# Optimization experiments

Hardware: AMD Instinct MI355X
Metric: run time of the kernel (lower is better)

## Reference

```python
import math
import jax, jax.numpy as jnp
import numpy as np

B, S, D, H = 2, 2048, 1024, 16
HD = D // H
I = 3752  # round(1024 * 11/3 / 8) * 8, per GluMLP default
EPS = 1e-6


def _alibi_bias(nheads, n):
    # AlibiPostionEmbedding: slopes (power-of-2 formula) * -1, times |i-j|
    start = 2.0 ** (-(2.0 ** (-(math.log2(nheads) - 3))))
    slopes = np.array([start * start ** i for i in range(nheads)], dtype=np.float64) * -1.0
    pos = np.arange(n)
    rel = np.abs(pos[None, :] - pos[:, None])  # [n, n]
    return jnp.asarray(slopes[:, None, None] * rel[None, :, :], dtype=jnp.float32)


def rmsnorm(h, w):
    h32 = h.astype(jnp.float32)
    var = jnp.mean(h32 * h32, axis=-1, keepdims=True)
    return (w * (h32 * jax.lax.rsqrt(var + EPS))).astype(h.dtype)


def setup_inputs() -> dict:
    key = jax.random.key(0)
    ks = jax.random.split(key, 16)
    sd = 1.0 / math.sqrt(D)
    si = 1.0 / math.sqrt(I)
    rn = lambda k, shape, s: jax.random.normal(k, shape, jnp.float32) * s
    return {
        "x": rn(ks[0], (B, S, D), 1.0),
        "wq": rn(ks[1], (D, D), sd), "bq": rn(ks[2], (D,), 0.02),
        "wk": rn(ks[3], (D, D), sd), "bk": rn(ks[4], (D,), 0.02),
        "wv": rn(ks[5], (D, D), sd), "bv": rn(ks[6], (D,), 0.02),
        "wo": rn(ks[7], (D, D), sd), "bo": rn(ks[8], (D,), 0.02),
        "w_gate": rn(ks[9], (D, I), sd),
        "w_up": rn(ks[10], (D, I), sd),
        "w_down": rn(ks[11], (I, D), si),
        "ln1_w": jnp.ones((D,), jnp.float32),
        "ln2_w": jnp.ones((D,), jnp.float32),
        "attn_bias": _alibi_bias(H, S),                       # [H, S, S]
        "tgt_mask": jnp.triu(jnp.ones((S, S), bool), 1),      # causal, True = masked
        "key_padding_mask": jnp.zeros((B, S), bool),          # True = padded
    }


def reference(x, wq, bq, wk, bk, wv, bv, wo, bo, w_gate, w_up, w_down,
              ln1_w, ln2_w, attn_bias, tgt_mask, key_padding_mask):
    # ---- TransformerEncoderLayer.forward (eval mode: dropout = identity) ----
    residual = x
    h = rmsnorm(x, ln1_w)
    # MultiheadAttention with ALiBi bias + fused bool masks
    q = (h @ wq + bq).reshape(B, S, H, HD)
    k = (h @ wk + bk).reshape(B, S, H, HD)
    v = (h @ wv + bv).reshape(B, S, H, HD)
    scores = jnp.einsum("bqhd,bkhd->bhqk", q, k) * (HD ** -0.5)  # [B,H,S,S]
    scores = scores + attn_bias[None]
    mask = tgt_mask[None, :, :] | key_padding_mask[:, None, :]   # [B,S,S]
    scores = jnp.where(mask[:, None, :, :], -jnp.inf, scores)
    probs = jax.nn.softmax(scores, axis=-1)
    attn = jnp.einsum("bhqk,bkhd->bqhd", probs, v).reshape(B, S, D)
    attn = attn @ wo + bo
    residual = attn + residual
    # GluMLP (SwiGLU)
    h2 = rmsnorm(residual, ln2_w)
    mlp = (jax.nn.silu(h2 @ w_gate) * (h2 @ w_up)) @ w_down
    return mlp + residual
```

## Files before the change

kernel.cpp:

```cpp
#include <hip/hip_runtime.h>
#include <hip/hip_bf16.h>
#include <cmath>

typedef __bf16 bf16_t;
typedef __bf16 bf16x8 __attribute__((ext_vector_type(8)));
typedef short  s16x8  __attribute__((ext_vector_type(8)));
typedef float  f32x4  __attribute__((ext_vector_type(4)));

static constexpr int Bn  = 2;
static constexpr int Sn  = 2048;
static constexpr int Dn  = 1024;
static constexpr int Hn  = 16;
static constexpr int In  = 3752;
static constexpr int Mn  = Bn * Sn;
static constexpr int Ipad = 3840;

__device__ __forceinline__ void cp16(const bf16_t* g, bf16_t* l) {
  __builtin_amdgcn_global_load_lds(
      (const __attribute__((address_space(1))) unsigned int*)g,
      (__attribute__((address_space(3))) unsigned int*)l, 16, 0, 0);
}

__global__ __launch_bounds__(256) void k_transpose(const float* __restrict__ in,
                                                   bf16_t* __restrict__ out,
                                                   int R, int C) {
  __shared__ float tile[32][33];
  const int c0 = blockIdx.x * 32, r0 = blockIdx.y * 32;
  const int tx = threadIdx.x & 31, ty = threadIdx.x >> 5;
#pragma unroll
  for (int e = 0; e < 4; ++e) {
    int r = r0 + ty + e * 8, c = c0 + tx;
    if (r < R && c < C) tile[ty + e * 8][tx] = in[(size_t)r * C + c];
  }
  __syncthreads();
#pragma unroll
  for (int e = 0; e < 4; ++e) {
    int c = c0 + ty + e * 8, r = r0 + tx;
    if (r < R && c < C) out[(size_t)c * R + r] = (bf16_t)tile[tx][ty + e * 8];
  }
}

__global__ __launch_bounds__(256) void k_rmsnorm(const float* __restrict__ in,
                                                 const float* __restrict__ w,
                                                 bf16_t* __restrict__ out) {
  const int row = blockIdx.x;
  const int tid = threadIdx.x;
  const float* ip = in + (size_t)row * Dn;
  float v[4];
  float ss = 0.f;
#pragma unroll
  for (int e = 0; e < 4; ++e) {
    v[e] = ip[tid + e * 256];
    ss += v[e] * v[e];
  }
  for (int off = 32; off > 0; off >>= 1) ss += __shfl_down(ss, off);
  __shared__ float red[4];
  if ((tid & 63) == 0) red[tid >> 6] = ss;
  __syncthreads();
  float tot = red[0] + red[1] + red[2] + red[3];
  float sc = rsqrtf(tot * (1.0f / Dn) + 1e-6f);
  bf16_t* op = out + (size_t)row * Dn;
#pragma unroll
  for (int e = 0; e < 4; ++e) {
    int idx = tid + e * 256;
    op[idx] = (bf16_t)(w[idx] * v[e] * sc);
  }
}

__global__ __launch_bounds__(256) void k_gemm64(
    const bf16_t* __restrict__ A, const bf16_t* __restrict__ Bt,
    const float* __restrict__ bias, const float* __restrict__ resid,
    float* __restrict__ outf, int N, int K, int lda, int ldb) {
  __shared__ bf16_t As[64 * 64];
  __shared__ bf16_t Bs[128 * 64];
  const int m0 = blockIdx.x * 64, n0 = blockIdx.y * 128;
  const int tid = threadIdx.x;
  const int lane = tid & 63, wid = tid >> 6;
  const int wc = wid * 32;
  const int l15 = lane & 15, quad = lane >> 4;
  const int sw = l15 & 7;
  const int srow_lo = lane >> 3, pchunk = lane & 7;

  f32x4 acc[4][2];
  const f32x4 z4 = {0.f, 0.f, 0.f, 0.f};
#pragma unroll
  for (int i = 0; i < 4; ++i)
#pragma unroll
    for (int j = 0; j < 2; ++j) acc[i][j] = z4;

  for (int k0 = 0; k0 < K; k0 += 64) {
#pragma unroll
    for (int c = 0; c < 2; ++c) {
      const int r = (wid * 2 + c) * 8 + srow_lo;
      const int gc = pchunk ^ (r & 7);
      cp16(A + (size_t)(m0 + r) * lda + k0 + gc * 8, As + (wid * 2 + c) * 512);
    }
#pragma unroll
    for (int c = 0; c < 4; ++c) {
      const int r = (wid * 4 + c) * 8 + srow_lo;
      const int gc = pchunk ^ (r & 7);
      cp16(Bt + (size_t)(n0 + r) * ldb + k0 + gc * 8, Bs + (wid * 4 + c) * 512);
    }
    __syncthreads();
#pragma unroll
    for (int kh = 0; kh < 2; ++kh) {
      const int ph = ((kh * 4 + quad) ^ sw) * 8;
      bf16x8 af[4], bfr[2];
#pragma unroll
      for (int i = 0; i < 4; ++i)
        af[i] = *(const bf16x8*)(As + (i * 16 + l15) * 64 + ph);
#pragma unroll
      for (int j = 0; j < 2; ++j)
        bfr[j] = *(const bf16x8*)(Bs + (wc + j * 16 + l15) * 64 + ph);
#pragma unroll
      for (int i = 0; i < 4; ++i)
#pragma unroll
        for (int j = 0; j < 2; ++j)
          acc[i][j] = __builtin_amdgcn_mfma_f32_16x16x32_bf16(af[i], bfr[j], acc[i][j], 0, 0, 0);
    }
    __syncthreads();
  }

#pragma unroll
  for (int i = 0; i < 4; ++i)
#pragma unroll
    for (int j = 0; j < 2; ++j) {
      const int col = n0 + wc + j * 16 + l15;
      const float bval = bias ? bias[col] : 0.f;
#pragma unroll
      for (int r = 0; r < 4; ++r) {
        const int row = m0 + i * 16 + quad * 4 + r;
        const size_t idx = (size_t)row * N + col;
        outf[idx] = acc[i][j][r] + bval + (resid ? resid[idx] : 0.f);
      }
    }
}

__global__ __launch_bounds__(256) void k_gemm_qkv(
    const bf16_t* __restrict__ A, const bf16_t* __restrict__ Bt,
    const float* __restrict__ bq, const float* __restrict__ bk,
    const float* __restrict__ bv,
    bf16_t* __restrict__ qk, bf16_t* __restrict__ vt) {
  __shared__ bf16_t As[128 * 64];
  __shared__ bf16_t Bs[128 * 64];
  const int m0 = blockIdx.x * 128, n0 = blockIdx.y * 128;
  const int tid = threadIdx.x;
  const int lane = tid & 63, wid = tid >> 6;
  const int wr = (wid >> 1) * 64, wc = (wid & 1) * 64;
  const int l15 = lane & 15, quad = lane >> 4;
  const int sw = l15 & 7;
  const int srow_lo = lane >> 3, pchunk = lane & 7;

  f32x4 acc[4][4];
  const f32x4 z4 = {0.f, 0.f, 0.f, 0.f};
#pragma unroll
  for (int i = 0; i < 4; ++i)
#pragma unroll
    for (int j = 0; j < 4; ++j) acc[i][j] = z4;

  for (int k0 = 0; k0 < Dn; k0 += 64) {
#pragma unroll
    for (int c = 0; c < 4; ++c) {
      const int r = (wid * 4 + c) * 8 + srow_lo;
      const int gc = pchunk ^ (r & 7);
      cp16(A  + (size_t)(m0 + r) * Dn + k0 + gc * 8, As + (wid * 4 + c) * 512);
      cp16(Bt + (size_t)(n0 + r) * Dn + k0 + gc * 8, Bs + (wid * 4 + c) * 512);
    }
    __syncthreads();
#pragma unroll
    for (int kh = 0; kh < 2; ++kh) {
      bf16x8 af[4], bfr[4];
      const int ph = ((kh * 4 + quad) ^ sw) * 8;
#pragma unroll
      for (int i = 0; i < 4; ++i)
        af[i] = *(const bf16x8*)(As + (wr + i * 16 + l15) * 64 + ph);
#pragma unroll
      for (int j = 0; j < 4; ++j)
        bfr[j] = *(const bf16x8*)(Bs + (wc + j * 16 + l15) * 64 + ph);
#pragma unroll
      for (int i = 0; i < 4; ++i)
#pragma unroll
        for (int j = 0; j < 4; ++j)
          acc[i][j] = __builtin_amdgcn_mfma_f32_16x16x32_bf16(af[i], bfr[j], acc[i][j], 0, 0, 0);
    }
    __syncthreads();
  }

#pragma unroll
  for (int i = 0; i < 4; ++i)
#pragma unroll
    for (int j = 0; j < 4; ++j) {
      const int col = n0 + wc + j * 16 + l15;
      const int sel = col >> 10;
      const float bval = (sel == 0) ? bq[col] : (sel == 1) ? bk[col - 1024] : bv[col - 2048];
#pragma unroll
      for (int r = 0; r < 4; ++r) {
        const int row = m0 + wr + i * 16 + quad * 4 + r;
        const float v = acc[i][j][r] + bval;
        if (sel < 2) {
          qk[(size_t)row * 2048 + col] = (bf16_t)v;
        } else {
          const int dd = col & 63, hh = (col >> 6) & 15;
          const int bb = row >> 11, ss = row & 2047;
          vt[(size_t)((bb * 16 + hh) * 64 + dd) * 2048 + ss] = (bf16_t)v;
        }
      }
    }
}

__global__ __launch_bounds__(256) void k_gemm_gateup(
    const bf16_t* __restrict__ A, const bf16_t* __restrict__ Bg,
    const bf16_t* __restrict__ Bu, bf16_t* __restrict__ out, int N, int ldo) {
  __shared__ bf16_t As[128 * 64];
  __shared__ bf16_t Gs[128 * 64];
  __shared__ bf16_t Us[128 * 64];
  const int m0 = blockIdx.x * 128, n0 = blockIdx.y * 128;
  const int tid = threadIdx.x;
  const int lane = tid & 63, wid = tid >> 6;
  const int wr = (wid >> 1) * 64, wc = (wid & 1) * 64;
  const int l15 = lane & 15, quad = lane >> 4;
  const int sw = l15 & 7;
  const int srow_lo = lane >> 3, pchunk = lane & 7;

  f32x4 accg[4][4], accu[4][4];
  const f32x4 z4 = {0.f, 0.f, 0.f, 0.f};
#pragma unroll
  for (int i = 0; i < 4; ++i)
#pragma unroll
    for (int j = 0; j < 4; ++j) { accg[i][j] = z4; accu[i][j] = z4; }

  for (int k0 = 0; k0 < Dn; k0 += 64) {
#pragma unroll
    for (int c = 0; c < 4; ++c) {
      const int r = (wid * 4 + c) * 8 + srow_lo;
      const int gc = pchunk ^ (r & 7);
      const int nb = min(n0 + r, N - 1);
      cp16(A  + (size_t)(m0 + r) * Dn + k0 + gc * 8, As + (wid * 4 + c) * 512);
      cp16(Bg + (size_t)nb * Dn + k0 + gc * 8, Gs + (wid * 4 + c) * 512);
      cp16(Bu + (size_t)nb * Dn + k0 + gc * 8, Us + (wid * 4 + c) * 512);
    }
    __syncthreads();
#pragma unroll
    for (int kh = 0; kh < 2; ++kh) {
      bf16x8 af[4], gf[4], uf[4];
      const int ph = ((kh * 4 + quad) ^ sw) * 8;
#pragma unroll
      for (int i = 0; i < 4; ++i)
        af[i] = *(const bf16x8*)(As + (wr + i * 16 + l15) * 64 + ph);
#pragma unroll
      for (int j = 0; j < 4; ++j) {
        gf[j] = *(const bf16x8*)(Gs + (wc + j * 16 + l15) * 64 + ph);
        uf[j] = *(const bf16x8*)(Us + (wc + j * 16 + l15) * 64 + ph);
      }
#pragma unroll
      for (int i = 0; i < 4; ++i)
#pragma unroll
        for (int j = 0; j < 4; ++j) {
          accg[i][j] = __builtin_amdgcn_mfma_f32_16x16x32_bf16(af[i], gf[j], accg[i][j], 0, 0, 0);
          accu[i][j] = __builtin_amdgcn_mfma_f32_16x16x32_bf16(af[i], uf[j], accu[i][j], 0, 0, 0);
        }
    }
    __syncthreads();
  }

#pragma unroll
  for (int i = 0; i < 4; ++i)
#pragma unroll
    for (int j = 0; j < 4; ++j) {
      const int col = n0 + wc + j * 16 + l15;
#pragma unroll
      for (int r = 0; r < 4; ++r) {
        const int row = m0 + wr + i * 16 + quad * 4 + r;
        const float g = accg[i][j][r];
        const float u = accu[i][j][r];
        const float sl = g / (1.f + expf(-g));
        out[(size_t)row * ldo + col] = (col < N) ? (bf16_t)(sl * u) : (bf16_t)0.f;
      }
    }
}

__global__ __launch_bounds__(256) void k_attn(
    const bf16_t* __restrict__ qk, const bf16_t* __restrict__ vt,
    bf16_t* __restrict__ Ob) {
  const int qt = (int)gridDim.x - 1 - (int)blockIdx.x;
  const int h  = blockIdx.y;
  const int b  = blockIdx.z;
  constexpr int LDK = 72;
  constexpr int LDP = 76;
  __shared__ bf16_t Ks[64 * LDK];
  __shared__ bf16_t Vt[64 * LDK];
  __shared__ bf16_t Ps[4][16 * LDP];

  const int tid  = threadIdx.x;
  const int lane = tid & 63, w = tid >> 6;
  const int l15  = lane & 15, quad = lane >> 4;

  constexpr float L2E = 1.4426950408889634f;
  const float slopeL = -exp2f(-0.5f * (float)(h + 1)) * L2E;

  const int qrow_frag = qt * 64 + w * 16 + l15;
  const size_t qbase = (size_t)(b * Sn + qrow_frag) * 2048 + h * 64;
  bf16x8 aq0 = *(const bf16x8*)(qk + qbase + quad * 8);
  bf16x8 aq1 = *(const bf16x8*)(qk + qbase + 32 + quad * 8);
#pragma unroll
  for (int e = 0; e < 8; ++e) {
    aq0[e] = (bf16_t)((float)aq0[e] * 0.125f);
    aq1[e] = (bf16_t)((float)aq1[e] * 0.125f);
  }

  const int qrow0 = qt * 64 + w * 16 + quad * 4;
  float Atr[4][4];
#pragma unroll
  for (int t = 0; t < 4; ++t)
#pragma unroll
    for (int rr = 0; rr < 4; ++rr)
      Atr[t][rr] = slopeL * (float)(qrow0 + rr - (t * 16 + l15));
  const float kstepL = slopeL * 64.f;

  f32x4 o[4], lacc;
  const f32x4 z4 = {0.f, 0.f, 0.f, 0.f};
#pragma unroll
  for (int dt = 0; dt < 4; ++dt) o[dt] = z4;
  lacc = z4;
  bf16x8 ones;
#pragma unroll
  for (int e = 0; e < 8; ++e) ones[e] = (bf16_t)1.0f;

  const int r = tid >> 2, c0e = (tid & 3) * 16;
  const size_t kbase = (size_t)(b * Sn + r) * 2048 + 1024 + h * 64 + c0e;
  const size_t vbase = (size_t)((b * 16 + h) * 64 + r) * 2048 + c0e;

  s16x8 kr0 = *(const s16x8*)(qk + kbase);
  s16x8 kr1 = *(const s16x8*)(qk + kbase + 8);
  s16x8 vr0 = *(const s16x8*)(vt + vbase);
  s16x8 vr1 = *(const s16x8*)(vt + vbase + 8);

  const int nkt = qt + 1;
  for (int kt = 0; kt < nkt; ++kt) {
    __syncthreads();
    *(s16x8*)(Ks + r * LDK + c0e)     = kr0;
    *(s16x8*)(Ks + r * LDK + c0e + 8) = kr1;
    *(s16x8*)(Vt + r * LDK + c0e)     = vr0;
    *(s16x8*)(Vt + r * LDK + c0e + 8) = vr1;
    __syncthreads();
    if (kt + 1 < nkt) {
      const size_t gkn = kbase + (size_t)(kt + 1) * (64 * 2048);
      kr0 = *(const s16x8*)(qk + gkn);
      kr1 = *(const s16x8*)(qk + gkn + 8);
      const size_t gvn = vbase + (size_t)(kt + 1) * 64;
      vr0 = *(const s16x8*)(vt + gvn);
      vr1 = *(const s16x8*)(vt + gvn + 8);
    }

    f32x4 s[4];
#pragma unroll
    for (int t = 0; t < 4; ++t) s[t] = z4;
#pragma unroll
    for (int t = 0; t < 4; ++t) {
      bf16x8 bk0 = *(const bf16x8*)(Ks + (t * 16 + l15) * LDK + quad * 8);
      bf16x8 bk1 = *(const bf16x8*)(Ks + (t * 16 + l15) * LDK + 32 + quad * 8);
      s[t] = __builtin_amdgcn_mfma_f32_16x16x32_bf16(aq0, bk0, s[t], 0, 0, 0);
      s[t] = __builtin_amdgcn_mfma_f32_16x16x32_bf16(aq1, bk1, s[t], 0, 0, 0);
    }

    const float ko = kstepL * (float)kt;
    const bool diag = (kt == qt);
#pragma unroll
    for (int t = 0; t < 4; ++t) {
      const int j = kt * 64 + t * 16 + l15;
#pragma unroll
      for (int rr = 0; rr < 4; ++rr) {
        float v2 = fmaf(s[t][rr], L2E, Atr[t][rr] - ko);
        if (diag && j > qrow0 + rr) v2 = -3.0e38f;
        Ps[w][(quad * 4 + rr) * LDP + t * 16 + l15] = (bf16_t)exp2f(v2);
      }
    }

#pragma unroll
    for (int kh = 0; kh < 2; ++kh) {
      bf16x8 pa = *(const bf16x8*)(Ps[w] + l15 * LDP + kh * 32 + quad * 8);
      lacc = __builtin_amdgcn_mfma_f32_16x16x32_bf16(pa, ones, lacc, 0, 0, 0);
#pragma unroll
      for (int dt = 0; dt < 4; ++dt) {
        bf16x8 bv = *(const bf16x8*)(Vt + (dt * 16 + l15) * LDK + kh * 32 + quad * 8);
        o[dt] = __builtin_amdgcn_mfma_f32_16x16x32_bf16(pa, bv, o[dt], 0, 0, 0);
      }
    }
  }

#pragma unroll
  for (int rr = 0; rr < 4; ++rr) {
    const float inv = 1.f / lacc[rr];
    bf16_t* op = Ob + ((size_t)(b * Sn + qrow0 + rr) * Hn + h) * 64;
#pragma unroll
    for (int dt = 0; dt < 4; ++dt)
      op[dt * 16 + l15] = (bf16_t)(o[dt][rr] * inv);
  }
}

extern "C" void kernel_launch(void* const* d_in, const int* in_sizes, int n_in,
                              void* d_out, int out_size, void* d_ws, size_t ws_size,
                              hipStream_t stream) {
  (void)in_sizes; (void)n_in; (void)out_size; (void)ws_size;
  const float* x   = (const float*)d_in[0];
  const float* wq  = (const float*)d_in[1];
  const float* bq  = (const float*)d_in[2];
  const float* wk_ = (const float*)d_in[3];
  const float* bk  = (const float*)d_in[4];
  const float* wv  = (const float*)d_in[5];
  const float* bv  = (const float*)d_in[6];
  const float* wo  = (const float*)d_in[7];
  const float* bo  = (const float*)d_in[8];
  const float* wg  = (const float*)d_in[9];
  const float* wu  = (const float*)d_in[10];
  const float* wd  = (const float*)d_in[11];
  const float* ln1 = (const float*)d_in[12];
  const float* ln2 = (const float*)d_in[13];

  char* base = (char*)d_ws;
  const size_t MiB = 1024 * 1024;
  bf16_t* h1     = (bf16_t*)(base);
  bf16_t* wqkvT  = (bf16_t*)(base + 8 * MiB);
  bf16_t* qkb    = (bf16_t*)(base + 16 * MiB);
  float*  res1   = (float*) (base + 16 * MiB);
  bf16_t* vt     = (bf16_t*)(base + 32 * MiB);
  bf16_t* mlp    = (bf16_t*)(base + 40 * MiB);
  bf16_t* wgT    = h1;
  bf16_t* woT    = wqkvT;
  bf16_t* wuT    = wqkvT;
  bf16_t* wdT    = vt;
  bf16_t* attnb  = (bf16_t*)d_out;
  bf16_t* h2     = (bf16_t*)d_out;

  const dim3 blk(256);
  const dim3 gT(Dn / 32, Dn / 32);

  k_rmsnorm<<<dim3(Mn), blk, 0, stream>>>(x, ln1, h1);

  k_transpose<<<gT, blk, 0, stream>>>(wq,  wqkvT, Dn, Dn);
  k_transpose<<<gT, blk, 0, stream>>>(wk_, wqkvT + (size_t)Dn * Dn, Dn, Dn);
  k_transpose<<<gT, blk, 0, stream>>>(wv,  wqkvT + 2 * (size_t)Dn * Dn, Dn, Dn);

  k_gemm_qkv<<<dim3(Mn / 128, 3072 / 128), blk, 0, stream>>>(h1, wqkvT, bq, bk, bv, qkb, vt);

  k_attn<<<dim3(Sn / 64, Hn, Bn), blk, 0, stream>>>(qkb, vt, attnb);

  k_transpose<<<gT, blk, 0, stream>>>(wo, woT, Dn, Dn);
  k_gemm64<<<dim3(Mn / 64, Dn / 128), blk, 0, stream>>>(
      attnb, woT, bo, x, res1, Dn, Dn, Dn, Dn);

  k_rmsnorm<<<dim3(Mn), blk, 0, stream>>>(res1, ln2, h2);

  k_transpose<<<dim3((In + 31) / 32, Dn / 32), blk, 0, stream>>>(wg, wgT, Dn, In);
  k_transpose<<<dim3((In + 31) / 32, Dn / 32), blk, 0, stream>>>(wu, wuT, Dn, In);
  k_transpose<<<dim3(Dn / 32, (In + 31) / 32), blk, 0, stream>>>(wd, wdT, In, Dn);

  k_gemm_gateup<<<dim3(Mn / 128, Ipad / 128), blk, 0, stream>>>(
      h2, wgT, wuT, mlp, In, Ipad);

  k_gemm64<<<dim3(Mn / 64, Dn / 128), blk, 0, stream>>>(
      mlp, wdT, nullptr, res1, (float*)d_out, Dn, Ipad, Ipad, In);
}
```

Measured before the change: 743.9 us.

## Batch weight transposes, store V row-major, and widen attention query tile to 128

All seven weight transposes are merged into one launch over a 3D grid, with separate workspace buffers so they no longer alias. The QKV GEMM now writes a plain row-major [M,3072] buffer instead of scattering V into a transposed layout, and the attention kernel transposes V into shared memory itself. Each attention block now handles 128 query rows (two 16-row groups per wave), so every K/V tile loaded is reused twice as much, at the cost of more registers, half as many blocks, and scalar strided LDS writes for the V transpose. The merged transpose grid also launches many blocks that exit early.

```diff
diff --git a/kernel.cpp b/kernel.cpp
--- a/kernel.cpp
+++ b/kernel.cpp
@@ -21,22 +21,25 @@
       (__attribute__((address_space(3))) unsigned int*)l, 16, 0, 0);
 }
 
-__global__ __launch_bounds__(256) void k_transpose(const float* __restrict__ in,
-                                                   bf16_t* __restrict__ out,
-                                                   int R, int C) {
+struct TransJob  { const float* src; bf16_t* dst; int R, C; };
+struct TransJobs { TransJob j[7]; };
+
+__global__ __launch_bounds__(256) void k_transpose_all(TransJobs jobs) {
+  const TransJob jb = jobs.j[blockIdx.z];
+  const int c0 = blockIdx.x * 32, r0 = blockIdx.y * 32;
+  if (c0 >= jb.C || r0 >= jb.R) return;
   __shared__ float tile[32][33];
-  const int c0 = blockIdx.x * 32, r0 = blockIdx.y * 32;
   const int tx = threadIdx.x & 31, ty = threadIdx.x >> 5;
 #pragma unroll
   for (int e = 0; e < 4; ++e) {
     int r = r0 + ty + e * 8, c = c0 + tx;
-    if (r < R && c < C) tile[ty + e * 8][tx] = in[(size_t)r * C + c];
+    if (r < jb.R && c < jb.C) tile[ty + e * 8][tx] = jb.src[(size_t)r * jb.C + c];
   }
   __syncthreads();
 #pragma unroll
   for (int e = 0; e < 4; ++e) {
     int c = c0 + ty + e * 8, r = r0 + tx;
-    if (r < R && c < C) out[(size_t)c * R + r] = (bf16_t)tile[tx][ty + e * 8];
+    if (r < jb.R && c < jb.C) jb.dst[(size_t)c * jb.R + r] = (bf16_t)tile[tx][ty + e * 8];
   }
 }
 
@@ -139,8 +142,7 @@
 __global__ __launch_bounds__(256) void k_gemm_qkv(
     const bf16_t* __restrict__ A, const bf16_t* __restrict__ Bt,
     const float* __restrict__ bq, const float* __restrict__ bk,
-    const float* __restrict__ bv,
-    bf16_t* __restrict__ qk, bf16_t* __restrict__ vt) {
+    const float* __restrict__ bv, bf16_t* __restrict__ qkvb) {
   __shared__ bf16_t As[128 * 64];
   __shared__ bf16_t Bs[128 * 64];
   const int m0 = blockIdx.x * 128, n0 = blockIdx.y * 128;
@@ -196,14 +198,7 @@
 #pragma unroll
       for (int r = 0; r < 4; ++r) {
         const int row = m0 + wr + i * 16 + quad * 4 + r;
-        const float v = acc[i][j][r] + bval;
-        if (sel < 2) {
-          qk[(size_t)row * 2048 + col] = (bf16_t)v;
-        } else {
-          const int dd = col & 63, hh = (col >> 6) & 15;
-          const int bb = row >> 11, ss = row & 2047;
-          vt[(size_t)((bb * 16 + hh) * 64 + dd) * 2048 + ss] = (bf16_t)v;
-        }
+        qkvb[(size_t)row * 3072 + col] = (bf16_t)(acc[i][j][r] + bval);
       }
     }
 }
@@ -280,16 +275,14 @@
 }
 
 __global__ __launch_bounds__(256) void k_attn(
-    const bf16_t* __restrict__ qk, const bf16_t* __restrict__ vt,
-    bf16_t* __restrict__ Ob) {
+    const bf16_t* __restrict__ qkv, bf16_t* __restrict__ Ob) {
   const int qt = (int)gridDim.x - 1 - (int)blockIdx.x;
   const int h  = blockIdx.y;
   const int b  = blockIdx.z;
-  constexpr int LDK = 72;
-  constexpr int LDP = 76;
+  constexpr int LDK = 72, LDP = 76;
   __shared__ bf16_t Ks[64 * LDK];
   __shared__ bf16_t Vt[64 * LDK];
-  __shared__ bf16_t Ps[4][16 * LDP];
+  __shared__ bf16_t Ps[4][32 * LDP];
 
   const int tid  = threadIdx.x;
   const int lane = tid & 63, w = tid >> 6;
@@ -298,104 +291,127 @@
   constexpr float L2E = 1.4426950408889634f;
   const float slopeL = -exp2f(-0.5f * (float)(h + 1)) * L2E;
 
-  const int qrow_frag = qt * 64 + w * 16 + l15;
-  const size_t qbase = (size_t)(b * Sn + qrow_frag) * 2048 + h * 64;
-  bf16x8 aq0 = *(const bf16x8*)(qk + qbase + quad * 8);
-  bf16x8 aq1 = *(const bf16x8*)(qk + qbase + 32 + quad * 8);
-#pragma unroll
-  for (int e = 0; e < 8; ++e) {
-    aq0[e] = (bf16_t)((float)aq0[e] * 0.125f);
-    aq1[e] = (bf16_t)((float)aq1[e] * 0.125f);
-  }
-
-  const int qrow0 = qt * 64 + w * 16 + quad * 4;
-  float Atr[4][4];
-#pragma unroll
-  for (int t = 0; t < 4; ++t)
-#pragma unroll
-    for (int rr = 0; rr < 4; ++rr)
-      Atr[t][rr] = slopeL * (float)(qrow0 + rr - (t * 16 + l15));
-  const float kstepL = slopeL * 64.f;
-
-  f32x4 o[4], lacc;
+  bf16x8 aq[2][2];
+#pragma unroll
+  for (int g = 0; g < 2; ++g) {
+    const int row = qt * 128 + w * 32 + g * 16 + l15;
+    const bf16_t* qp = qkv + (size_t)(b * Sn + row) * 3072 + h * 64;
+    aq[g][0] = *(const bf16x8*)(qp + quad * 8);
+    aq[g][1] = *(const bf16x8*)(qp + 32 + quad * 8);
+#pragma unroll
+    for (int e = 0; e < 8; ++e) {
+      aq[g][0][e] = (bf16_t)((float)aq[g][0][e] * 0.125f);
+      aq[g][1][e] = (bf16_t)((float)aq[g][1][e] * 0.125f);
+    }
+  }
+
+  int qrow[2];
+  float rowterm[2][4];
+#pragma unroll
+  for (int g = 0; g < 2; ++g) {
+    qrow[g] = qt * 128 + w * 32 + g * 16 + quad * 4;
+#pragma unroll
+    for (int rr = 0; rr < 4; ++rr) rowterm[g][rr] = slopeL * (float)(qrow[g] + rr);
+  }
+  float colbase[4];
+#pragma unroll
+  for (int t = 0; t < 4; ++t) colbase[t] = slopeL * (float)(t * 16 + l15);
+
+  f32x4 o[2][4], lacc[2];
   const f32x4 z4 = {0.f, 0.f, 0.f, 0.f};
 #pragma unroll
-  for (int dt = 0; dt < 4; ++dt) o[dt] = z4;
-  lacc = z4;
+  for (int g = 0; g < 2; ++g) {
+    lacc[g] = z4;
+#pragma unroll
+    for (int dt = 0; dt < 4; ++dt) o[g][dt] = z4;
+  }
   bf16x8 ones;
 #pragma unroll
   for (int e = 0; e < 8; ++e) ones[e] = (bf16_t)1.0f;
 
   const int r = tid >> 2, c0e = (tid & 3) * 16;
-  const size_t kbase = (size_t)(b * Sn + r) * 2048 + 1024 + h * 64 + c0e;
-  const size_t vbase = (size_t)((b * 16 + h) * 64 + r) * 2048 + c0e;
-
-  s16x8 kr0 = *(const s16x8*)(qk + kbase);
-  s16x8 kr1 = *(const s16x8*)(qk + kbase + 8);
-  s16x8 vr0 = *(const s16x8*)(vt + vbase);
-  s16x8 vr1 = *(const s16x8*)(vt + vbase + 8);
-
-  const int nkt = qt + 1;
+  const size_t kbase = (size_t)(b * Sn + r) * 3072 + 1024 + h * 64 + c0e;
+  const size_t step  = (size_t)64 * 3072;
+
+  s16x8 kr0 = *(const s16x8*)(qkv + kbase);
+  s16x8 kr1 = *(const s16x8*)(qkv + kbase + 8);
+  s16x8 vr0 = *(const s16x8*)(qkv + kbase + 1024);
+  s16x8 vr1 = *(const s16x8*)(qkv + kbase + 1024 + 8);
+
+  const int nkt = 2 * qt + 2;
   for (int kt = 0; kt < nkt; ++kt) {
     __syncthreads();
     *(s16x8*)(Ks + r * LDK + c0e)     = kr0;
     *(s16x8*)(Ks + r * LDK + c0e + 8) = kr1;
-    *(s16x8*)(Vt + r * LDK + c0e)     = vr0;
-    *(s16x8*)(Vt + r * LDK + c0e + 8) = vr1;
+    {
+      const bf16x8 v0 = *(const bf16x8*)&vr0, v1 = *(const bf16x8*)&vr1;
+#pragma unroll
+      for (int e = 0; e < 8; ++e) {
+        Vt[(c0e + e) * LDK + r]     = v0[e];
+        Vt[(c0e + 8 + e) * LDK + r] = v1[e];
+      }
+    }
     __syncthreads();
     if (kt + 1 < nkt) {
-      const size_t gkn = kbase + (size_t)(kt + 1) * (64 * 2048);
-      kr0 = *(const s16x8*)(qk + gkn);
-      kr1 = *(const s16x8*)(qk + gkn + 8);
-      const size_t gvn = vbase + (size_t)(kt + 1) * 64;
-      vr0 = *(const s16x8*)(vt + gvn);
-      vr1 = *(const s16x8*)(vt + gvn + 8);
-    }
-
-    f32x4 s[4];
-#pragma unroll
-    for (int t = 0; t < 4; ++t) s[t] = z4;
-#pragma unroll
-    for (int t = 0; t < 4; ++t) {
-      bf16x8 bk0 = *(const bf16x8*)(Ks + (t * 16 + l15) * LDK + quad * 8);
-      bf16x8 bk1 = *(const bf16x8*)(Ks + (t * 16 + l15) * LDK + 32 + quad * 8);
-      s[t] = __builtin_amdgcn_mfma_f32_16x16x32_bf16(aq0, bk0, s[t], 0, 0, 0);
-      s[t] = __builtin_amdgcn_mfma_f32_16x16x32_bf16(aq1, bk1, s[t], 0, 0, 0);
-    }
-
-    const float ko = kstepL * (float)kt;
-    const bool diag = (kt == qt);
-#pragma unroll
-    for (int t = 0; t < 4; ++t) {
-      const int j = kt * 64 + t * 16 + l15;
-#pragma unroll
-      for (int rr = 0; rr < 4; ++rr) {
-        float v2 = fmaf(s[t][rr], L2E, Atr[t][rr] - ko);
-        if (diag && j > qrow0 + rr) v2 = -3.0e38f;
-        Ps[w][(quad * 4 + rr) * LDP + t * 16 + l15] = (bf16_t)exp2f(v2);
-      }
-    }
-
-#pragma unroll
-    for (int kh = 0; kh < 2; ++kh) {
-      bf16x8 pa = *(const bf16x8*)(Ps[w] + l15 * LDP + kh * 32 + quad * 8);
-      lacc = __builtin_amdgcn_mfma_f32_16x16x32_bf16(pa, ones, lacc, 0, 0, 0);
-#pragma unroll
-      for (int dt = 0; dt < 4; ++dt) {
-        bf16x8 bv = *(const bf16x8*)(Vt + (dt * 16 + l15) * LDK + kh * 32 + quad * 8);
-        o[dt] = __builtin_amdgcn_mfma_f32_16x16x32_bf16(pa, bv, o[dt], 0, 0, 0);
-      }
-    }
-  }
-
-#pragma unroll
-  for (int rr = 0; rr < 4; ++rr) {
-    const float inv = 1.f / lacc[rr];
-    bf16_t* op = Ob + ((size_t)(b * Sn + qrow0 + rr) * Hn + h) * 64;
-#pragma unroll
-    for (int dt = 0; dt < 4; ++dt)
-      op[dt * 16 + l15] = (bf16_t)(o[dt][rr] * inv);
-  }
+      const size_t kb = kbase + (size_t)(kt + 1) * step;
+      kr0 = *(const s16x8*)(qkv + kb);
+      kr1 = *(const s16x8*)(qkv + kb + 8);
+      vr0 = *(const s16x8*)(qkv + kb + 1024);
+      vr1 = *(const s16x8*)(qkv + kb + 1024 + 8);
+    }
+
+    const float kofs = slopeL * (float)(kt * 64);
+    const bool diag = (kt + 2 >= nkt);
+
+#pragma unroll
+    for (int g = 0; g < 2; ++g) {
+      f32x4 s[4];
+#pragma unroll
+      for (int t = 0; t < 4; ++t) s[t] = z4;
+#pragma unroll
+      for (int t = 0; t < 4; ++t) {
+        bf16x8 bk0 = *(const bf16x8*)(Ks + (t * 16 + l15) * LDK + quad * 8);
+        bf16x8 bk1 = *(const bf16x8*)(Ks + (t * 16 + l15) * LDK + 32 + quad * 8);
+        s[t] = __builtin_amdgcn_mfma_f32_16x16x32_bf16(aq[g][0], bk0, s[t], 0, 0, 0);
+        s[t] = __builtin_amdgcn_mfma_f32_16x16x32_bf16(aq[g][1], bk1, s[t], 0, 0, 0);
+      }
+#pragma unroll
+      for (int t = 0; t < 4; ++t) {
+        const int j = kt * 64 + t * 16 + l15;
+#pragma unroll
+        for (int rr = 0; rr < 4; ++rr) {
+          float v2 = fmaf(s[t][rr], L2E, rowterm[g][rr] - (kofs + colbase[t]));
+          if (diag && j > qrow[g] + rr) v2 = -3.0e38f;
+          Ps[w][(g * 16 + quad * 4 + rr) * LDP + t * 16 + l15] = (bf16_t)exp2f(v2);
+        }
+      }
+    }
+
+#pragma unroll
+    for (int g = 0; g < 2; ++g) {
+#pragma unroll
+      for (int kh = 0; kh < 2; ++kh) {
+        bf16x8 pa = *(const bf16x8*)(Ps[w] + (g * 16 + l15) * LDP + kh * 32 + quad * 8);
+        lacc[g] = __builtin_amdgcn_mfma_f32_16x16x32_bf16(pa, ones, lacc[g], 0, 0, 0);
+#pragma unroll
+        for (int dt = 0; dt < 4; ++dt) {
+          bf16x8 bv = *(const bf16x8*)(Vt + (dt * 16 + l15) * LDK + kh * 32 + quad * 8);
+          o[g][dt] = __builtin_amdgcn_mfma_f32_16x16x32_bf16(pa, bv, o[g][dt], 0, 0, 0);
+        }
+      }
+    }
+  }
+
+#pragma unroll
+  for (int g = 0; g < 2; ++g)
+#pragma unroll
+    for (int rr = 0; rr < 4; ++rr) {
+      const float inv = 1.f / lacc[g][rr];
+      bf16_t* op = Ob + (size_t)(b * Sn + qrow[g] + rr) * 1024 + h * 64;
+#pragma unroll
+      for (int dt = 0; dt < 4; ++dt)
+        op[dt * 16 + l15] = (bf16_t)(o[g][dt][rr] * inv);
+    }
 }
 
 extern "C" void kernel_launch(void* const* d_in, const int* in_sizes, int n_in,
@@ -419,42 +435,41 @@
 
   char* base = (char*)d_ws;
   const size_t MiB = 1024 * 1024;
-  bf16_t* h1     = (bf16_t*)(base);
-  bf16_t* wqkvT  = (bf16_t*)(base + 8 * MiB);
-  bf16_t* qkb    = (bf16_t*)(base + 16 * MiB);
-  float*  res1   = (float*) (base + 16 * MiB);
-  bf16_t* vt     = (bf16_t*)(base + 32 * MiB);
-  bf16_t* mlp    = (bf16_t*)(base + 40 * MiB);
-  bf16_t* wgT    = h1;
-  bf16_t* woT    = wqkvT;
-  bf16_t* wuT    = wqkvT;
-  bf16_t* wdT    = vt;
-  bf16_t* attnb  = (bf16_t*)d_out;
-  bf16_t* h2     = (bf16_t*)d_out;
+  bf16_t* h1    = (bf16_t*)(base);
+  bf16_t* wqkvT = (bf16_t*)(base + 8  * MiB);
+  bf16_t* woT   = (bf16_t*)(base + 16 * MiB);
+  bf16_t* wgT   = (bf16_t*)(base + 24 * MiB);
+  bf16_t* wuT   = (bf16_t*)(base + 32 * MiB);
+  bf16_t* wdT   = (bf16_t*)(base + 40 * MiB);
+  bf16_t* qkvb  = (bf16_t*)(base + 48 * MiB);
+  float*  res1  = (float*) (base + 72 * MiB);
+  bf16_t* mlp   = (bf16_t*)(base + 88 * MiB);
+  bf16_t* attnb = (bf16_t*)d_out;
+  bf16_t* h2    = (bf16_t*)d_out;
 
   const dim3 blk(256);
-  const dim3 gT(Dn / 32, Dn / 32);
+
+  TransJobs jobs;
+  jobs.j[0] = {wq,  wqkvT,                      Dn, Dn};
+  jobs.j[1] = {wk_, wqkvT + (size_t)Dn * Dn,    Dn, Dn};
+  jobs.j[2] = {wv,  wqkvT + 2 * (size_t)Dn * Dn, Dn, Dn};
+  jobs.j[3] = {wo,  woT, Dn, Dn};
+  jobs.j[4] = {wg,  wgT, Dn, In};
+  jobs.j[5] = {wu,  wuT, Dn, In};
+  jobs.j[6] = {wd,  wdT, In, Dn};
+  k_transpose_all<<<dim3(118, 118, 7), blk, 0, stream>>>(jobs);
 
   k_rmsnorm<<<dim3(Mn), blk, 0, stream>>>(x, ln1, h1);
 
-  k_transpose<<<gT, blk, 0, stream>>>(wq,  wqkvT, Dn, Dn);
-  k_transpose<<<gT, blk, 0, stream>>>(wk_, wqkvT + (size_t)Dn * Dn, Dn, Dn);
-  k_transpose<<<gT, blk, 0, stream>>>(wv,  wqkvT + 2 * (size_t)Dn * Dn, Dn, Dn);
-
-  k_gemm_qkv<<<dim3(Mn / 128, 3072 / 128), blk, 0, stream>>>(h1, wqkvT, bq, bk, bv, qkb, vt);
-
-  k_attn<<<dim3(Sn / 64, Hn, Bn), blk, 0, stream>>>(qkb, vt, attnb);
-
-  k_transpose<<<gT, blk, 0, stream>>>(wo, woT, Dn, Dn);
+  k_gemm_qkv<<<dim3(Mn / 128, 3072 / 128), blk, 0, stream>>>(h1, wqkvT, bq, bk, bv, qkvb);
+
+  k_attn<<<dim3(Sn / 128, Hn, Bn), blk, 0, stream>>>(qkvb, attnb);
+
   k_gemm64<<<dim3(Mn / 64, Dn / 128), blk, 0, stream>>>(
       attnb, woT, bo, x, res1, Dn, Dn, Dn, Dn);
 
   k_rmsnorm<<<dim3(Mn), blk, 0, stream>>>(res1, ln2, h2);
 
-  k_transpose<<<dim3((In + 31) / 32, Dn / 32), blk, 0, stream>>>(wg, wgT, Dn, In);
-  k_transpose<<<dim3((In + 31) / 32, Dn / 32), blk, 0, stream>>>(wu, wuT, Dn, In);
-  k_transpose<<<dim3(Dn / 32, (In + 31) / 32), blk, 0, stream>>>(wd, wdT, In, Dn);
-
   k_gemm_gateup<<<dim3(Mn / 128, Ipad / 128), blk, 0, stream>>>(
       h2, wgT, wuT, mlp, In, Ipad);
 
```

New measurement: 739.2 us. Within noise of the previous version (-0.6%).
